# Kernel tuning notes

Hardware: AMD Instinct MI355X
Metric: run time of the kernel (lower is better)

The kernel has to match this reference:

```python
import jax, jax.numpy as jnp
import numpy as np


def _normal_distance(n1, n2):
    # Cosine-style normal distance: 1 - <n1, n2>. The original module stubs
    # this as 0; we use the canonical mesh-normal loss so the cdist+argmin+
    # gather chain is exercised end-to-end.
    return 1.0 - jnp.sum(n1 * n2, axis=-1)


def setup_inputs() -> dict:
    key = jax.random.key(0)
    k1, k2, k3, k4 = jax.random.split(key, 4)
    N, M = 8192, 32768
    pred_pts = jax.random.normal(k1, (1, N, 3), dtype=jnp.float32)
    pred_nrm = jax.random.normal(k2, (1, N, 3), dtype=jnp.float32)
    gt_pts = jax.random.normal(k3, (1, M, 3), dtype=jnp.float32)
    gt_nrm = jax.random.normal(k4, (1, M, 3), dtype=jnp.float32)
    # unit normals, as on a real mesh
    pred_nrm = pred_nrm / jnp.linalg.norm(pred_nrm, axis=-1, keepdims=True)
    gt_nrm = gt_nrm / jnp.linalg.norm(gt_nrm, axis=-1, keepdims=True)
    return {
        "predicted_points_batch": pred_pts,
        "predicted_normals_batch": pred_nrm,
        "gt_points_batch": gt_pts,
        "gt_normals_batch": gt_nrm,
    }


def reference(predicted_points_batch, predicted_normals_batch,
              gt_points_batch, gt_normals_batch):
    # Original forward returns inside the first loop iteration -> element 0 only.
    p = predicted_points_batch[0]    # [N,3]
    pn = predicted_normals_batch[0]  # [N,3]
    g = gt_points_batch[0]           # [M,3]
    gn = gt_normals_batch[0]         # [M,3]

    # Squared pairwise distances (monotone in true cdist; only argmin is used).
    # d2[i,j] = |p_i|^2 + |g_j|^2 - 2 p_i . g_j   -> one [N,M] intermediate.
    d2 = (jnp.sum(p * p, axis=1)[:, None]
          + jnp.sum(g * g, axis=1)[None, :]
          - 2.0 * (p @ g.T))                      # [N,M]

    gt_idx = jnp.argmin(d2, axis=1)    # nearest gt point per predicted point, [N]
    pr_idx = jnp.argmin(d2, axis=0)    # nearest predicted point per gt point, [M]

    nearest_gt_normals = gn[gt_idx]    # [N,3]
    nearest_pr_normals = pn[pr_idx]    # [M,3]

    dist1 = _normal_distance(pn, nearest_gt_normals)  # [N]
    dist2 = _normal_distance(gn, nearest_pr_normals)  # [M]
    return jnp.mean(dist1) + jnp.mean(dist2)
```

## Files before the change

kernel.cpp:

```cpp
#include <hip/hip_runtime.h>
#include <stdint.h>
#include <float.h>

#define BLK 256
#define IPT 8
#define OWNERS (BLK * IPT)
#define SLICE 128
#define SUB 64

typedef unsigned long long ull;

__device__ __forceinline__ unsigned int ford(float f) {
    int b = __float_as_int(f);
    return (b >= 0) ? ((unsigned)b ^ 0x80000000u) : ~(unsigned)b;
}
__device__ __forceinline__ float ford_inv(unsigned int u) {
    int b = (u & 0x80000000u) ? (int)(u ^ 0x80000000u) : (int)~u;
    return __int_as_float(b);
}

__device__ __forceinline__ float vmin(float a, float b) {
    float d;
    asm("v_min_f32 %0, %1, %2" : "=v"(d) : "v"(a), "v"(b));
    return d;
}

__global__ __launch_bounds__(BLK) void nn_min_dual(
    const float* __restrict__ p, const float* __restrict__ g,
    ull* __restrict__ rowmin, ull* __restrict__ colmin,
    int rowBlocks, int rowSlices, int colSlices)
{
    __shared__ float4 sb[SLICE];

    const float* A; const float* B; ull* outmin; int id, nSlices;
    if ((int)blockIdx.x < rowBlocks) {
        id = blockIdx.x;             A = p; B = g; outmin = rowmin; nSlices = rowSlices;
    } else {
        id = blockIdx.x - rowBlocks; A = g; B = p; outmin = colmin; nSlices = colSlices;
    }
    const int chunk = id / nSlices;
    const int slice = id - chunk * nSlices;
    const int s0 = slice * SLICE;

    if (threadIdx.x < SLICE) {
        int s = s0 + threadIdx.x;
        float bx = B[3 * s], by = B[3 * s + 1], bz = B[3 * s + 2];
        float w = fmaf(bz, bz, fmaf(by, by, bx * bx));
        sb[threadIdx.x] = make_float4(bx, by, bz, w);
    }

    const int o0 = chunk * OWNERS + threadIdx.x;
    float ax[IPT], ay[IPT], az[IPT], best[IPT];
    int base[IPT];
#pragma unroll
    for (int r = 0; r < IPT; ++r) {
        int o = o0 + r * BLK;
        ax[r] = -2.0f * A[3 * o];
        ay[r] = -2.0f * A[3 * o + 1];
        az[r] = -2.0f * A[3 * o + 2];
        best[r] = FLT_MAX;
        base[r] = s0;
    }
    __syncthreads();

    for (int st = 0; st < SLICE; st += SUB) {
        float prev[IPT];
#pragma unroll
        for (int r = 0; r < IPT; ++r) prev[r] = best[r];
#pragma unroll 4
        for (int k = st; k < st + SUB; ++k) {
            float4 q = sb[k];
#pragma unroll
            for (int r = 0; r < IPT; ++r) {
                float v = fmaf(ax[r], q.x, fmaf(ay[r], q.y, fmaf(az[r], q.z, q.w)));
                best[r] = vmin(best[r], v);
            }
        }
#pragma unroll
        for (int r = 0; r < IPT; ++r)
            if (best[r] < prev[r]) base[r] = s0 + st;
    }

#pragma unroll
    for (int r = 0; r < IPT; ++r) {
        ull packed = ((ull)ford(best[r]) << 32) | (unsigned)base[r];
        atomicMin(&outmin[o0 + r * BLK], packed);
    }
}

__global__ __launch_bounds__(BLK) void finalize_kernel(
    const ull* __restrict__ rowmin, const ull* __restrict__ colmin,
    const float* __restrict__ p, const float* __restrict__ g,
    const float* __restrict__ pn, const float* __restrict__ gn,
    float* __restrict__ out, int N, int M, float invN, float invM)
{
    int t = blockIdx.x * BLK + threadIdx.x;
    float c = 0.0f;
    if (t < N + M) {
        const float* A; const float* B; const float* An; const float* Bn;
        ull packed; int o; float inv;
        if (t < N) { o = t;     A = p; B = g; An = pn; Bn = gn; packed = rowmin[o]; inv = invN; }
        else       { o = t - N; A = g; B = p; An = gn; Bn = pn; packed = colmin[o]; inv = invM; }

        float ax = -2.0f * A[3 * o];
        float ay = -2.0f * A[3 * o + 1];
        float az = -2.0f * A[3 * o + 2];
        float bestf = ford_inv((unsigned int)(packed >> 32));
        int base = (int)(packed & 0xffffffffull);

        int idx = 0x7fffffff;
#pragma unroll 8
        for (int j = 0; j < SUB; ++j) {
            int s = base + j;
            float bx = B[3 * s], by = B[3 * s + 1], bz = B[3 * s + 2];
            float w = fmaf(bz, bz, fmaf(by, by, bx * bx));
            float v = fmaf(ax, bx, fmaf(ay, by, fmaf(az, bz, w)));
            idx = min(idx, (v == bestf) ? s : 0x7fffffff);
        }

        float d = An[3 * o] * Bn[3 * idx] + An[3 * o + 1] * Bn[3 * idx + 1]
                + An[3 * o + 2] * Bn[3 * idx + 2];
        c = (1.0f - d) * inv;
    }
#pragma unroll
    for (int off = 32; off > 0; off >>= 1) c += __shfl_down(c, off, 64);
    __shared__ float partial[BLK / 64];
    if ((threadIdx.x & 63) == 0) partial[threadIdx.x >> 6] = c;
    __syncthreads();
    if (threadIdx.x == 0) {
        float s = 0.0f;
#pragma unroll
        for (int w = 0; w < BLK / 64; ++w) s += partial[w];
        atomicAdd(out, s);
    }
}

extern "C" void kernel_launch(void* const* d_in, const int* in_sizes, int n_in,
                              void* d_out, int out_size, void* d_ws, size_t ws_size,
                              hipStream_t stream) {
    const float* p  = (const float*)d_in[0];
    const float* pn = (const float*)d_in[1];
    const float* g  = (const float*)d_in[2];
    const float* gn = (const float*)d_in[3];
    const int N = in_sizes[0] / 3;
    const int M = in_sizes[2] / 3;

    ull* rowmin = (ull*)d_ws;
    ull* colmin = rowmin + N;
    float* out = (float*)d_out;

    hipMemsetAsync(d_ws, 0xFF, (size_t)(N + M) * sizeof(ull), stream);
    hipMemsetAsync(d_out, 0, sizeof(float), stream);

    const int rowSlices = M / SLICE;
    const int colSlices = N / SLICE;
    const int rowBlocks = (N / OWNERS) * rowSlices;
    const int colBlocks = (M / OWNERS) * colSlices;
    nn_min_dual<<<rowBlocks + colBlocks, BLK, 0, stream>>>(
        p, g, rowmin, colmin, rowBlocks, rowSlices, colSlices);

    int tot = N + M;
    finalize_kernel<<<(tot + BLK - 1) / BLK, BLK, 0, stream>>>(
        rowmin, colmin, p, g, pn, gn, out, N, M, 1.0f / N, 1.0f / M);
}
```

Before: 116.0 us.

## Prefetch LDS points, wave-parallel index recovery, single memset with last-block finalize

The inner distance loop now software-pipelines LDS reads by loading the next four points while computing on the current four. The per-point atomicMin is replaced by atomicMax on the complemented key, which lets a single zero memset initialize both the workspace and the new accumulator and done counter, dropping the second memset. The finalize kernel assigns one wavefront per point: 64 lanes each recheck one candidate in the 64-wide sub-slice and a ballot picks the first match, replacing the serial 64-iteration loop per thread. A last-block-done pattern writes the final sum. This adds atomic and fence overhead and leaves 63 of 64 lanes idle during the normal dot product.

```diff
diff --git a/kernel.cpp b/kernel.cpp
--- a/kernel.cpp
+++ b/kernel.cpp
@@ -18,7 +18,6 @@
     int b = (u & 0x80000000u) ? (int)(u ^ 0x80000000u) : (int)~u;
     return __int_as_float(b);
 }
-
 __device__ __forceinline__ float vmin(float a, float b) {
     float d;
     asm("v_min_f32 %0, %1, %2" : "=v"(d) : "v"(a), "v"(b));
@@ -67,14 +66,33 @@
         float prev[IPT];
 #pragma unroll
         for (int r = 0; r < IPT; ++r) prev[r] = best[r];
-#pragma unroll 4
-        for (int k = st; k < st + SUB; ++k) {
-            float4 q = sb[k];
+
+        float4 p0 = sb[st], p1 = sb[st + 1], p2 = sb[st + 2], p3 = sb[st + 3];
+#pragma unroll 2
+        for (int k = st; k < st + SUB; k += 4) {
+            int kn = min(k + 4, SLICE - 4);
+            float4 n0 = sb[kn], n1 = sb[kn + 1], n2 = sb[kn + 2], n3 = sb[kn + 3];
 #pragma unroll
             for (int r = 0; r < IPT; ++r) {
-                float v = fmaf(ax[r], q.x, fmaf(ay[r], q.y, fmaf(az[r], q.z, q.w)));
+                float v = fmaf(ax[r], p0.x, fmaf(ay[r], p0.y, fmaf(az[r], p0.z, p0.w)));
                 best[r] = vmin(best[r], v);
             }
+#pragma unroll
+            for (int r = 0; r < IPT; ++r) {
+                float v = fmaf(ax[r], p1.x, fmaf(ay[r], p1.y, fmaf(az[r], p1.z, p1.w)));
+                best[r] = vmin(best[r], v);
+            }
+#pragma unroll
+            for (int r = 0; r < IPT; ++r) {
+                float v = fmaf(ax[r], p2.x, fmaf(ay[r], p2.y, fmaf(az[r], p2.z, p2.w)));
+                best[r] = vmin(best[r], v);
+            }
+#pragma unroll
+            for (int r = 0; r < IPT; ++r) {
+                float v = fmaf(ax[r], p3.x, fmaf(ay[r], p3.y, fmaf(az[r], p3.z, p3.w)));
+                best[r] = vmin(best[r], v);
+            }
+            p0 = n0; p1 = n1; p2 = n2; p3 = n3;
         }
 #pragma unroll
         for (int r = 0; r < IPT; ++r)
@@ -84,7 +102,7 @@
 #pragma unroll
     for (int r = 0; r < IPT; ++r) {
         ull packed = ((ull)ford(best[r]) << 32) | (unsigned)base[r];
-        atomicMin(&outmin[o0 + r * BLK], packed);
+        atomicMax(&outmin[o0 + r * BLK], ~packed);
     }
 }
 
@@ -92,46 +110,58 @@
     const ull* __restrict__ rowmin, const ull* __restrict__ colmin,
     const float* __restrict__ p, const float* __restrict__ g,
     const float* __restrict__ pn, const float* __restrict__ gn,
-    float* __restrict__ out, int N, int M, float invN, float invM)
+    float* __restrict__ out, float* __restrict__ accum,
+    unsigned int* __restrict__ done,
+    int N, int M, float invN, float invM)
 {
-    int t = blockIdx.x * BLK + threadIdx.x;
-    float c = 0.0f;
-    if (t < N + M) {
+    const int lane = threadIdx.x & 63;
+    const int wid  = (blockIdx.x * BLK + threadIdx.x) >> 6;
+    const int nw   = (gridDim.x * BLK) >> 6;
+
+    float wsum = 0.0f;
+    for (int o = wid; o < N + M; o += nw) {
         const float* A; const float* B; const float* An; const float* Bn;
-        ull packed; int o; float inv;
-        if (t < N) { o = t;     A = p; B = g; An = pn; Bn = gn; packed = rowmin[o]; inv = invN; }
-        else       { o = t - N; A = g; B = p; An = gn; Bn = pn; packed = colmin[o]; inv = invM; }
-
-        float ax = -2.0f * A[3 * o];
-        float ay = -2.0f * A[3 * o + 1];
-        float az = -2.0f * A[3 * o + 2];
-        float bestf = ford_inv((unsigned int)(packed >> 32));
+        ull stored; int oo; float inv;
+        if (o < N) { oo = o;     A = p; B = g; An = pn; Bn = gn; stored = rowmin[oo]; inv = invN; }
+        else       { oo = o - N; A = g; B = p; An = gn; Bn = pn; stored = colmin[oo]; inv = invM; }
+        ull packed = ~stored;
+        float bestv = ford_inv((unsigned int)(packed >> 32));
         int base = (int)(packed & 0xffffffffull);
 
-        int idx = 0x7fffffff;
-#pragma unroll 8
-        for (int j = 0; j < SUB; ++j) {
-            int s = base + j;
-            float bx = B[3 * s], by = B[3 * s + 1], bz = B[3 * s + 2];
-            float w = fmaf(bz, bz, fmaf(by, by, bx * bx));
-            float v = fmaf(ax, bx, fmaf(ay, by, fmaf(az, bz, w)));
-            idx = min(idx, (v == bestf) ? s : 0x7fffffff);
+        int s = base + lane;
+        float bx = B[3 * s], by = B[3 * s + 1], bz = B[3 * s + 2];
+        float w = fmaf(bz, bz, fmaf(by, by, bx * bx));
+        float ax = -2.0f * A[3 * oo];
+        float ay = -2.0f * A[3 * oo + 1];
+        float az = -2.0f * A[3 * oo + 2];
+        float v = fmaf(ax, bx, fmaf(ay, by, fmaf(az, bz, w)));
+
+        ull mask = __ballot(v == bestv);
+        int bit = mask ? (__ffsll(mask) - 1) : 0;
+        int j = base + bit;
+
+        if (lane == 0) {
+            float d = An[3 * oo] * Bn[3 * j] + An[3 * oo + 1] * Bn[3 * j + 1]
+                    + An[3 * oo + 2] * Bn[3 * j + 2];
+            wsum += (1.0f - d) * inv;
         }
+    }
 
-        float d = An[3 * o] * Bn[3 * idx] + An[3 * o + 1] * Bn[3 * idx + 1]
-                + An[3 * o + 2] * Bn[3 * idx + 2];
-        c = (1.0f - d) * inv;
-    }
-#pragma unroll
-    for (int off = 32; off > 0; off >>= 1) c += __shfl_down(c, off, 64);
-    __shared__ float partial[BLK / 64];
-    if ((threadIdx.x & 63) == 0) partial[threadIdx.x >> 6] = c;
+    __shared__ float part[BLK / 64];
+    if (lane == 0) part[threadIdx.x >> 6] = wsum;
     __syncthreads();
     if (threadIdx.x == 0) {
         float s = 0.0f;
 #pragma unroll
-        for (int w = 0; w < BLK / 64; ++w) s += partial[w];
-        atomicAdd(out, s);
+        for (int w = 0; w < BLK / 64; ++w) s += part[w];
+        atomicAdd(accum, s);
+        __threadfence();
+        unsigned int c = atomicAdd(done, 1u);
+        if (c == gridDim.x - 1) {
+            __threadfence();
+            float tot = atomicAdd(accum, 0.0f);
+            out[0] = tot;
+        }
     }
 }
 
@@ -147,10 +177,11 @@
 
     ull* rowmin = (ull*)d_ws;
     ull* colmin = rowmin + N;
+    float* accum = (float*)(colmin + M);
+    unsigned int* done = (unsigned int*)(accum + 1);
     float* out = (float*)d_out;
 
-    hipMemsetAsync(d_ws, 0xFF, (size_t)(N + M) * sizeof(ull), stream);
-    hipMemsetAsync(d_out, 0, sizeof(float), stream);
+    hipMemsetAsync(d_ws, 0, (size_t)(N + M) * sizeof(ull) + 16, stream);
 
     const int rowSlices = M / SLICE;
     const int colSlices = N / SLICE;
@@ -159,7 +190,6 @@
     nn_min_dual<<<rowBlocks + colBlocks, BLK, 0, stream>>>(
         p, g, rowmin, colmin, rowBlocks, rowSlices, colSlices);
 
-    int tot = N + M;
-    finalize_kernel<<<(tot + BLK - 1) / BLK, BLK, 0, stream>>>(
-        rowmin, colmin, p, g, pn, gn, out, N, M, 1.0f / N, 1.0f / M);
+    finalize_kernel<<<640, BLK, 0, stream>>>(
+        rowmin, colmin, p, g, pn, gn, out, accum, done, N, M, 1.0f / N, 1.0f / M);
 }
```

Measured after the change: 133.2 us. +14.8%, slower.
